# Optimization experiments

Hardware: AMD Instinct MI355X
Metric: run time of the kernel (lower is better)

The kernel has to match this reference:

```python
import jax, jax.numpy as jnp
import numpy as np

RADIUS = 0.4   # 0.2 * nlayer, nlayer = 2
NSAMPLE = 32   # k


def _fps(xyz, m):
    """Farthest point sampling. xyz: (B, N, 3) -> idx (B, m) int32.
    Matches pointnet2 CUDA kernel: first sampled point is index 0."""
    B, N, _ = xyz.shape

    def step(carry, _):
        dist, far = carry
        centroid = jnp.take_along_axis(xyz, far[:, None, None], axis=1)  # (B,1,3)
        d = jnp.sum((xyz - centroid) ** 2, axis=-1)                      # (B,N)
        dist = jnp.minimum(dist, d)
        return (dist, jnp.argmax(dist, axis=-1).astype(jnp.int32)), far

    init = (jnp.full((B, N), jnp.inf, dtype=xyz.dtype),
            jnp.zeros((B,), dtype=jnp.int32))
    _, idx = jax.lax.scan(step, init, None, length=m)  # (m, B)
    return idx.T                                       # (B, m)


def _ball_query(radius, k, xyz, new_xyz):
    """xyz (B,N,3), new_xyz (B,M,3) -> (B,M,k) int32.
    First k in-radius indices in ascending index order; slots past the
    number of in-radius points are filled with the first found index
    (pointnet2 ball_query semantics)."""
    N = xyz.shape[1]
    d2 = jnp.sum((new_xyz[:, :, None, :] - xyz[:, None, :, :]) ** 2, axis=-1)  # (B,M,N)
    key = jnp.where(d2 < radius * radius,
                    jnp.arange(N, dtype=jnp.int32), jnp.int32(N))              # (B,M,N)
    topv, _ = jax.lax.top_k(-key, k)   # k smallest keys, ascending
    idx = -topv                        # (B,M,k)
    valid = idx < N
    idx = jnp.where(valid, idx, idx[..., :1])  # pad with first found index
    return idx


def _group(t, idx):
    """t (B,C,N), idx (B,M,k) -> (B,C,M,k)."""
    return jnp.take_along_axis(t[:, :, None, :], idx[:, None, :, :], axis=3)


def setup_inputs() -> dict:
    key = jax.random.key(0)
    k1, k2, k3 = jax.random.split(key, 3)
    return {
        "x": jax.random.normal(k1, (8, 3, 8192), dtype=jnp.float32),
        "feature": jax.random.normal(k2, (8, 64, 8192), dtype=jnp.float32),
        "weight": jax.random.normal(k3, (64, 64), dtype=jnp.float32) / 8.0,
        "num_pool": 2048,
    }


def reference(x, feature, weight, num_pool):
    # x: (B,3,N) coordinates, feature: (B,C,N), weight: 1x1 conv (C_out, C_in)
    xyz = jnp.transpose(x, (0, 2, 1))                       # (B,N,3)
    fps_idx = _fps(xyz, num_pool)                           # (B,M)
    new_xyz = jnp.take_along_axis(xyz, fps_idx[:, :, None], axis=1)  # (B,M,3)
    sub_idx = _ball_query(RADIUS, NSAMPLE, xyz, new_xyz)    # (B,M,k)

    x_out = _group(x, sub_idx).max(axis=-1)                 # (B,3,M)
    fg = _group(feature, sub_idx)                           # (B,C,M,k)
    f_out = jnp.einsum('oc,bcmk->bomk', weight, fg).max(axis=-1)  # (B,C,M)
    return x_out, f_out
```

## Files before the change

kernel.cpp:

```cpp
#include <hip/hip_runtime.h>
#include <cstdint>
#include <cstddef>

#define BB 8
#define NN 8192
#define CC 64
#define MM 2048
#define KK 32

typedef float vfloat2 __attribute__((ext_vector_type(2)));

__device__ __forceinline__ float sqdist_exact(float x, float y, float z,
                                              float cx, float cy, float cz) {
    float dx = __fsub_rn(x, cx);
    float dy = __fsub_rn(y, cy);
    float dz = __fsub_rn(z, cz);
    return __fadd_rn(__fadd_rn(__fmul_rn(dx, dx), __fmul_rn(dy, dy)),
                     __fmul_rn(dz, dz));
}

template <int CTRL>
__device__ __forceinline__ unsigned dpp_max_u32(unsigned v) {
    unsigned s = (unsigned)__builtin_amdgcn_update_dpp(0, (int)v, CTRL, 0xF, 0xF, true);
    return v > s ? v : s;
}
template <int CTRL>
__device__ __forceinline__ unsigned dpp_min_u32(unsigned v) {
    unsigned s = (unsigned)__builtin_amdgcn_update_dpp(0x7FFFFFFF, (int)v, CTRL, 0xF, 0xF, false);
    return v < s ? v : s;
}

__device__ __forceinline__ int octile(float v) {
    return (v > -1.1503494f) + (v > -0.6744898f) + (v > -0.3186394f) + (v > 0.0f) +
           (v > 0.3186394f) + (v > 0.6744898f) + (v > 1.1503494f);
}

__device__ __forceinline__ int morton9(int bx, int by, int bz) {
    int m = (bz & 1) | ((bz & 2) << 2) | ((bz & 4) << 4);
    m |= ((by & 1) << 1) | ((by & 2) << 3) | ((by & 4) << 5);
    m |= ((bx & 1) << 2) | ((bx & 2) << 4) | ((bx & 4) << 6);
    return m;
}

__global__ __launch_bounds__(512) void fps_kernel(const float* __restrict__ x,
                                                  int* __restrict__ fps_idx) {
#pragma clang fp contract(off)
    const int b = blockIdx.x;
    const int tid = threadIdx.x;
    const int lane = tid & 63;
    const float* xb = x + (size_t)b * 3 * NN;
    int* fps_store = fps_idx + b * MM;

    __shared__ float sx[NN];
    __shared__ float sy[NN];
    __shared__ float sz[NN];
    __shared__ int sidx[NN];
    __shared__ int hist[512];
    __shared__ int scanb[512];
    __shared__ int sfps[MM];
    __shared__ unsigned long long red3[3];

    const vfloat2* gx = (const vfloat2*)xb;
    const vfloat2* gy = (const vfloat2*)(xb + NN);
    const vfloat2* gz = (const vfloat2*)(xb + 2 * NN);

    vfloat2 lx[8], ly[8], lz[8];
#pragma unroll
    for (int p = 0; p < 8; ++p) {
        const int e = tid + p * 512;
        lx[p] = gx[e];
        ly[p] = gy[e];
        lz[p] = gz[e];
        ((vfloat2*)sx)[e] = lx[p];
        ((vfloat2*)sy)[e] = ly[p];
        ((vfloat2*)sz)[e] = lz[p];
    }
    hist[tid] = 0;
    if (tid < 3) red3[tid] = 0ull;
    __syncthreads();

    int mybin[16];
#pragma unroll
    for (int p = 0; p < 8; ++p) {
        int b0 = morton9(octile(lx[p].x), octile(ly[p].x), octile(lz[p].x));
        int b1 = morton9(octile(lx[p].y), octile(ly[p].y), octile(lz[p].y));
        mybin[2 * p] = b0;
        mybin[2 * p + 1] = b1;
        atomicAdd(&hist[b0], 1);
        atomicAdd(&hist[b1], 1);
    }
    __syncthreads();
    int own = hist[tid];
    scanb[tid] = own;
    __syncthreads();
    for (int off = 1; off < 512; off <<= 1) {
        int add = (tid >= off) ? scanb[tid - off] : 0;
        __syncthreads();
        scanb[tid] += add;
        __syncthreads();
    }
    hist[tid] = scanb[tid] - own;
    __syncthreads();
#pragma unroll
    for (int p = 0; p < 8; ++p) {
        const int i0 = 2 * (tid + p * 512);
        int pos0 = atomicAdd(&hist[mybin[2 * p]], 1);
        sidx[pos0] = i0;
        int pos1 = atomicAdd(&hist[mybin[2 * p + 1]], 1);
        sidx[pos1] = i0 + 1;
    }
    __syncthreads();

    vfloat2 px[8], py[8], pz[8], dist[8];
    int idxr[16];
#pragma unroll
    for (int p = 0; p < 8; ++p) {
        const int j0 = sidx[tid * 16 + 2 * p];
        const int j1 = sidx[tid * 16 + 2 * p + 1];
        idxr[2 * p] = j0;
        idxr[2 * p + 1] = j1;
        px[p] = (vfloat2){sx[j0], sx[j1]};
        py[p] = (vfloat2){sy[j0], sy[j1]};
        pz[p] = (vfloat2){sz[j0], sz[j1]};
        dist[p] = (vfloat2){INFINITY, INFINITY};
    }
    float blx = fminf(px[0].x, px[0].y), bhx = fmaxf(px[0].x, px[0].y);
    float bly = fminf(py[0].x, py[0].y), bhy = fmaxf(py[0].x, py[0].y);
    float blz = fminf(pz[0].x, pz[0].y), bhz = fmaxf(pz[0].x, pz[0].y);
#pragma unroll
    for (int p = 1; p < 8; ++p) {
        blx = fminf(blx, fminf(px[p].x, px[p].y));
        bhx = fmaxf(bhx, fmaxf(px[p].x, px[p].y));
        bly = fminf(bly, fminf(py[p].x, py[p].y));
        bhy = fmaxf(bhy, fmaxf(py[p].x, py[p].y));
        blz = fminf(blz, fminf(pz[p].x, pz[p].y));
        bhz = fmaxf(bhz, fmaxf(pz[p].x, pz[p].y));
    }

    float cmax = INFINITY;
    int cidx = idxr[0];
    int far = 0;
    for (int t = 0; t < MM; ++t) {
        if (tid == 0) {
            sfps[t] = far;
            red3[(t + 1) % 3] = 0ull;
        }
        const float cx = sx[far];
        const float cy = sy[far];
        const float cz = sz[far];

        float qx = cx - fminf(fmaxf(cx, blx), bhx);
        float qy = cy - fminf(fmaxf(cy, bly), bhy);
        float qz = cz - fminf(fmaxf(cz, blz), bhz);
        float bound = (qx * qx + qy * qy) + qz * qz;
        const bool act = !(bound * 0.999f >= cmax);
        if (act) {
            const vfloat2 cx2 = {cx, cx};
            const vfloat2 cy2 = {cy, cy};
            const vfloat2 cz2 = {cz, cz};
            float mv = -1.0f;
#pragma unroll
            for (int p = 0; p < 8; ++p) {
                vfloat2 dx = px[p] - cx2;
                vfloat2 dy = py[p] - cy2;
                vfloat2 dz = pz[p] - cz2;
                vfloat2 m1 = dx * dx;
                vfloat2 m2 = dy * dy;
                vfloat2 m3 = dz * dz;
                vfloat2 s = (m1 + m2) + m3;
                vfloat2 nd;
                nd.x = fminf(dist[p].x, s.x);
                nd.y = fminf(dist[p].y, s.y);
                dist[p] = nd;
                mv = fmaxf(fmaxf(mv, nd.x), nd.y);
            }
            int mi = 0x7FFFFFFF;
#pragma unroll
            for (int p = 0; p < 8; ++p) {
                mi = min(mi, (dist[p].x == mv) ? idxr[2 * p] : 0x7FFFFFFF);
                mi = min(mi, (dist[p].y == mv) ? idxr[2 * p + 1] : 0x7FFFFFFF);
            }
            cmax = mv;
            cidx = mi;
        }

        unsigned mvb = __float_as_uint(cmax);
        mvb = dpp_max_u32<0x111>(mvb);
        mvb = dpp_max_u32<0x112>(mvb);
        mvb = dpp_max_u32<0x114>(mvb);
        mvb = dpp_max_u32<0x118>(mvb);
        mvb = dpp_max_u32<0x142>(mvb);
        mvb = dpp_max_u32<0x143>(mvb);
        const unsigned wmax = (unsigned)__builtin_amdgcn_readlane((int)mvb, 63);
        unsigned midx = (__float_as_uint(cmax) == wmax) ? (unsigned)cidx : 0x7FFFFFFFu;
        midx = dpp_min_u32<0x111>(midx);
        midx = dpp_min_u32<0x112>(midx);
        midx = dpp_min_u32<0x114>(midx);
        midx = dpp_min_u32<0x118>(midx);
        midx = dpp_min_u32<0x142>(midx);
        midx = dpp_min_u32<0x143>(midx);
        if (lane == 63) {
            unsigned long long key =
                ((unsigned long long)wmax << 32) | (unsigned)(~midx);
            atomicMax(&red3[t % 3], key);
        }
        __syncthreads();
        far = (int)(~(unsigned)red3[t % 3]);
    }
    __syncthreads();
    for (int t = tid; t < MM; t += 512) fps_store[t] = sfps[t];
}

__global__ __launch_bounds__(256) void transform_kernel(const float* __restrict__ feature,
                                                        const float* __restrict__ weight,
                                                        float* __restrict__ g) {
    __shared__ float Wl[64 * 64];
    const int tid = threadIdx.x;
    for (int k = tid; k < 64 * 64; k += 256) Wl[k] = weight[k];
    __syncthreads();

    const int P = blockIdx.x * 256 + tid;
    const int b = P >> 13;
    const int n = P & (NN - 1);
    const float* fb = feature + (size_t)b * CC * NN + n;

    float fr[64];
#pragma unroll
    for (int c = 0; c < 64; ++c) fr[c] = fb[(size_t)c * NN];

    float* go = g + ((size_t)b << 19) + (size_t)n * 64;
    for (int o = 0; o < 64; o += 4) {
        const float* w0 = &Wl[o * 64];
        const float* w1 = w0 + 64;
        const float* w2 = w0 + 128;
        const float* w3 = w0 + 192;
        float a0 = 0.f, a1 = 0.f, a2 = 0.f, a3 = 0.f;
#pragma unroll
        for (int c = 0; c < 64; c += 4) {
            float4 v0 = *(const float4*)(w0 + c);
            float4 v1 = *(const float4*)(w1 + c);
            float4 v2 = *(const float4*)(w2 + c);
            float4 v3 = *(const float4*)(w3 + c);
            a0 += v0.x * fr[c] + v0.y * fr[c + 1] + v0.z * fr[c + 2] + v0.w * fr[c + 3];
            a1 += v1.x * fr[c] + v1.y * fr[c + 1] + v1.z * fr[c + 2] + v1.w * fr[c + 3];
            a2 += v2.x * fr[c] + v2.y * fr[c + 1] + v2.z * fr[c + 2] + v2.w * fr[c + 3];
            a3 += v3.x * fr[c] + v3.y * fr[c + 1] + v3.z * fr[c + 2] + v3.w * fr[c + 3];
        }
        float4 r;
        r.x = a0; r.y = a1; r.z = a2; r.w = a3;
        *(float4*)(go + o) = r;
    }
}

__global__ __launch_bounds__(256) void bq_kernel(const float* __restrict__ x,
                                                 const int* __restrict__ fps_idx,
                                                 int* __restrict__ sub_idx,
                                                 float* __restrict__ xout) {
    const float R2 = (float)(0.4 * 0.4);
    int gw = (int)((blockIdx.x * 256 + threadIdx.x) >> 6);
    const int lane = threadIdx.x & 63;
    gw = __builtin_amdgcn_readfirstlane(gw);
    const int b = gw >> 11;
    const int m = gw & (MM - 1);
    const float* xb = x + (size_t)b * 3 * NN;

    const int ctr = fps_idx[gw];
    const float cx = xb[ctr];
    const float cy = xb[NN + ctr];
    const float cz = xb[2 * NN + ctr];

    int* sid = sub_idx + (size_t)gw * KK;
    int found = 0;
    int first = 0;
    float mx = -INFINITY, my = -INFINITY, mz = -INFINITY;

    for (int base = 0; base < NN; base += 64) {
        const int i = base + lane;
        const float xx = xb[i];
        const float yy = xb[NN + i];
        const float zz = xb[2 * NN + i];
        const float d2 = sqdist_exact(xx, yy, zz, cx, cy, cz);
        const bool q = d2 < R2;
        const unsigned long long mask = __ballot(q);
        if (q) {
            int pos = found + (int)__popcll(mask & ((1ull << lane) - 1ull));
            if (pos < KK) {
                sid[pos] = i;
                mx = fmaxf(mx, xx);
                my = fmaxf(my, yy);
                mz = fmaxf(mz, zz);
            }
        }
        if (found == 0 && mask != 0ull) first = base + (int)__builtin_ctzll(mask);
        found += (int)__popcll(mask);
        if (found >= KK) break;
    }
    if (found < KK) {
        if (lane < KK - found) sid[found + lane] = first;
    }
#pragma unroll
    for (int off = 32; off >= 1; off >>= 1) {
        mx = fmaxf(mx, __shfl_xor(mx, off, 64));
        my = fmaxf(my, __shfl_xor(my, off, 64));
        mz = fmaxf(mz, __shfl_xor(mz, off, 64));
    }
    if (lane == 0) {
        xout[(size_t)b * 3 * MM + 0 * MM + m] = mx;
        xout[(size_t)b * 3 * MM + 1 * MM + m] = my;
        xout[(size_t)b * 3 * MM + 2 * MM + m] = mz;
    }
}

__global__ __launch_bounds__(256) void gather_kernel(const float* __restrict__ g,
                                                     const int* __restrict__ sub_idx,
                                                     float* __restrict__ fout) {
    int gw = (int)((blockIdx.x * 256 + threadIdx.x) >> 6);
    const int lane = threadIdx.x & 63;
    gw = __builtin_amdgcn_readfirstlane(gw);
    const int b = gw >> 11;
    const int m = gw & (MM - 1);
    const int* sid = sub_idx + (size_t)gw * KK;
    const float* gb = g + ((size_t)b << 19);
    float acc = -INFINITY;
#pragma unroll
    for (int j = 0; j < KK; ++j) {
        const int id = sid[j];
        acc = fmaxf(acc, gb[(size_t)id * 64 + lane]);
    }
    fout[((size_t)b << 17) + ((size_t)lane << 11) + m] = acc;
}

extern "C" void kernel_launch(void* const* d_in, const int* in_sizes, int n_in,
                              void* d_out, int out_size, void* d_ws, size_t ws_size,
                              hipStream_t stream) {
    const float* x = (const float*)d_in[0];
    const float* feature = (const float*)d_in[1];
    const float* weight = (const float*)d_in[2];

    float* out = (float*)d_out;
    float* xout = out;
    float* fout = out + BB * 3 * MM;

    char* ws = (char*)d_ws;
    int* fps_idx = (int*)ws;
    int* sub_idx = (int*)(ws + (size_t)BB * MM * 4);
    float* g = (float*)(ws + (size_t)BB * MM * 4 + (size_t)BB * MM * KK * 4);

    fps_kernel<<<BB, 512, 0, stream>>>(x, fps_idx);
    transform_kernel<<<(BB * NN) / 256, 256, 0, stream>>>(feature, weight, g);
    bq_kernel<<<(BB * MM * 64) / 256, 256, 0, stream>>>(x, fps_idx, sub_idx, xout);
    gather_kernel<<<(BB * MM * 64) / 256, 256, 0, stream>>>(g, sub_idx, fout);
}
```

Measured before the change: 1.923 ms.

## Shrink FPS block, pack xyz in LDS, fuse ball query with gather

The FPS kernel drops from 512 to 256 threads per block, so each thread holds 32 points and the per-iteration barrier covers fewer waves. Coordinates are packed as interleaved xyz in shared memory. The two-pass wave argmax is replaced by one 64-bit key max reduction done with DPP. Separately, the ball-query and feature-gather kernels are merged so neighbor indices stay in LDS instead of passing through global memory. The risks are higher register pressure from doubling per-thread point state and serial ALU work per FPS iteration, on a kernel that runs only 8 blocks.

```diff
diff --git a/kernel.cpp b/kernel.cpp
--- a/kernel.cpp
+++ b/kernel.cpp
@@ -20,14 +20,13 @@
 }
 
 template <int CTRL>
-__device__ __forceinline__ unsigned dpp_max_u32(unsigned v) {
-    unsigned s = (unsigned)__builtin_amdgcn_update_dpp(0, (int)v, CTRL, 0xF, 0xF, true);
-    return v > s ? v : s;
-}
-template <int CTRL>
-__device__ __forceinline__ unsigned dpp_min_u32(unsigned v) {
-    unsigned s = (unsigned)__builtin_amdgcn_update_dpp(0x7FFFFFFF, (int)v, CTRL, 0xF, 0xF, false);
-    return v < s ? v : s;
+__device__ __forceinline__ unsigned long long dpp_max_u64(unsigned long long key) {
+    int lo = (int)(unsigned)key;
+    int hi = (int)(unsigned)(key >> 32);
+    int slo = __builtin_amdgcn_update_dpp(0, lo, CTRL, 0xF, 0xF, true);
+    int shi = __builtin_amdgcn_update_dpp(0, hi, CTRL, 0xF, 0xF, true);
+    unsigned long long o = ((unsigned long long)(unsigned)shi << 32) | (unsigned)slo;
+    return o > key ? o : key;
 }
 
 __device__ __forceinline__ int octile(float v) {
@@ -42,7 +41,7 @@
     return m;
 }
 
-__global__ __launch_bounds__(512) void fps_kernel(const float* __restrict__ x,
+__global__ __launch_bounds__(256) void fps_kernel(const float* __restrict__ x,
                                                   int* __restrict__ fps_idx) {
 #pragma clang fp contract(off)
     const int b = blockIdx.x;
@@ -51,9 +50,7 @@
     const float* xb = x + (size_t)b * 3 * NN;
     int* fps_store = fps_idx + b * MM;
 
-    __shared__ float sx[NN];
-    __shared__ float sy[NN];
-    __shared__ float sz[NN];
+    __shared__ float spk[NN * 3];
     __shared__ int sidx[NN];
     __shared__ int hist[512];
     __shared__ int scanb[512];
@@ -64,71 +61,76 @@
     const vfloat2* gy = (const vfloat2*)(xb + NN);
     const vfloat2* gz = (const vfloat2*)(xb + 2 * NN);
 
-    vfloat2 lx[8], ly[8], lz[8];
-#pragma unroll
-    for (int p = 0; p < 8; ++p) {
-        const int e = tid + p * 512;
-        lx[p] = gx[e];
-        ly[p] = gy[e];
-        lz[p] = gz[e];
-        ((vfloat2*)sx)[e] = lx[p];
-        ((vfloat2*)sy)[e] = ly[p];
-        ((vfloat2*)sz)[e] = lz[p];
+#pragma unroll
+    for (int p = 0; p < 16; ++p) {
+        const int e = tid + p * 256;
+        vfloat2 ax = gx[e];
+        vfloat2 ay = gy[e];
+        vfloat2 az = gz[e];
+        spk[6 * e + 0] = ax.x;
+        spk[6 * e + 1] = ay.x;
+        spk[6 * e + 2] = az.x;
+        spk[6 * e + 3] = ax.y;
+        spk[6 * e + 4] = ay.y;
+        spk[6 * e + 5] = az.y;
     }
     hist[tid] = 0;
+    hist[tid + 256] = 0;
     if (tid < 3) red3[tid] = 0ull;
     __syncthreads();
 
-    int mybin[16];
-#pragma unroll
-    for (int p = 0; p < 8; ++p) {
-        int b0 = morton9(octile(lx[p].x), octile(ly[p].x), octile(lz[p].x));
-        int b1 = morton9(octile(lx[p].y), octile(ly[p].y), octile(lz[p].y));
-        mybin[2 * p] = b0;
-        mybin[2 * p + 1] = b1;
-        atomicAdd(&hist[b0], 1);
-        atomicAdd(&hist[b1], 1);
-    }
-    __syncthreads();
-    int own = hist[tid];
-    scanb[tid] = own;
+    int mybin[32];
+#pragma unroll
+    for (int p = 0; p < 32; ++p) {
+        const int i = tid + p * 256;
+        int bn = morton9(octile(spk[3 * i]), octile(spk[3 * i + 1]),
+                         octile(spk[3 * i + 2]));
+        mybin[p] = bn;
+        atomicAdd(&hist[bn], 1);
+    }
+    __syncthreads();
+    int own0 = hist[tid];
+    int own1 = hist[tid + 256];
+    scanb[tid] = own0;
+    scanb[tid + 256] = own1;
     __syncthreads();
     for (int off = 1; off < 512; off <<= 1) {
-        int add = (tid >= off) ? scanb[tid - off] : 0;
+        int a0 = (tid >= off) ? scanb[tid - off] : 0;
+        int a1 = (tid + 256 >= off) ? scanb[tid + 256 - off] : 0;
         __syncthreads();
-        scanb[tid] += add;
+        scanb[tid] += a0;
+        scanb[tid + 256] += a1;
         __syncthreads();
     }
-    hist[tid] = scanb[tid] - own;
-    __syncthreads();
-#pragma unroll
-    for (int p = 0; p < 8; ++p) {
-        const int i0 = 2 * (tid + p * 512);
-        int pos0 = atomicAdd(&hist[mybin[2 * p]], 1);
-        sidx[pos0] = i0;
-        int pos1 = atomicAdd(&hist[mybin[2 * p + 1]], 1);
-        sidx[pos1] = i0 + 1;
-    }
-    __syncthreads();
-
-    vfloat2 px[8], py[8], pz[8], dist[8];
-    int idxr[16];
-#pragma unroll
-    for (int p = 0; p < 8; ++p) {
-        const int j0 = sidx[tid * 16 + 2 * p];
-        const int j1 = sidx[tid * 16 + 2 * p + 1];
+    hist[tid] = scanb[tid] - own0;
+    hist[tid + 256] = scanb[tid + 256] - own1;
+    __syncthreads();
+#pragma unroll
+    for (int p = 0; p < 32; ++p) {
+        const int i = tid + p * 256;
+        int pos = atomicAdd(&hist[mybin[p]], 1);
+        sidx[pos] = i;
+    }
+    __syncthreads();
+
+    vfloat2 px[16], py[16], pz[16], dist[16];
+    int idxr[32];
+#pragma unroll
+    for (int p = 0; p < 16; ++p) {
+        const int j0 = sidx[tid * 32 + 2 * p];
+        const int j1 = sidx[tid * 32 + 2 * p + 1];
         idxr[2 * p] = j0;
         idxr[2 * p + 1] = j1;
-        px[p] = (vfloat2){sx[j0], sx[j1]};
-        py[p] = (vfloat2){sy[j0], sy[j1]};
-        pz[p] = (vfloat2){sz[j0], sz[j1]};
+        px[p] = (vfloat2){spk[3 * j0], spk[3 * j1]};
+        py[p] = (vfloat2){spk[3 * j0 + 1], spk[3 * j1 + 1]};
+        pz[p] = (vfloat2){spk[3 * j0 + 2], spk[3 * j1 + 2]};
         dist[p] = (vfloat2){INFINITY, INFINITY};
     }
     float blx = fminf(px[0].x, px[0].y), bhx = fmaxf(px[0].x, px[0].y);
     float bly = fminf(py[0].x, py[0].y), bhy = fmaxf(py[0].x, py[0].y);
     float blz = fminf(pz[0].x, pz[0].y), bhz = fmaxf(pz[0].x, pz[0].y);
 #pragma unroll
-    for (int p = 1; p < 8; ++p) {
+    for (int p = 1; p < 16; ++p) {
         blx = fminf(blx, fminf(px[p].x, px[p].y));
         bhx = fmaxf(bhx, fmaxf(px[p].x, px[p].y));
         bly = fminf(bly, fminf(py[p].x, py[p].y));
@@ -145,9 +147,9 @@
             sfps[t] = far;
             red3[(t + 1) % 3] = 0ull;
         }
-        const float cx = sx[far];
-        const float cy = sy[far];
-        const float cz = sz[far];
+        const float cx = spk[3 * far];
+        const float cy = spk[3 * far + 1];
+        const float cz = spk[3 * far + 2];
 
         float qx = cx - fminf(fmaxf(cx, blx), bhx);
         float qy = cy - fminf(fmaxf(cy, bly), bhy);
@@ -160,7 +162,7 @@
             const vfloat2 cz2 = {cz, cz};
             float mv = -1.0f;
 #pragma unroll
-            for (int p = 0; p < 8; ++p) {
+            for (int p = 0; p < 16; ++p) {
                 vfloat2 dx = px[p] - cx2;
                 vfloat2 dy = py[p] - cy2;
                 vfloat2 dz = pz[p] - cz2;
@@ -176,7 +178,7 @@
             }
             int mi = 0x7FFFFFFF;
 #pragma unroll
-            for (int p = 0; p < 8; ++p) {
+            for (int p = 0; p < 16; ++p) {
                 mi = min(mi, (dist[p].x == mv) ? idxr[2 * p] : 0x7FFFFFFF);
                 mi = min(mi, (dist[p].y == mv) ? idxr[2 * p + 1] : 0x7FFFFFFF);
             }
@@ -184,31 +186,21 @@
             cidx = mi;
         }
 
-        unsigned mvb = __float_as_uint(cmax);
-        mvb = dpp_max_u32<0x111>(mvb);
-        mvb = dpp_max_u32<0x112>(mvb);
-        mvb = dpp_max_u32<0x114>(mvb);
-        mvb = dpp_max_u32<0x118>(mvb);
-        mvb = dpp_max_u32<0x142>(mvb);
-        mvb = dpp_max_u32<0x143>(mvb);
-        const unsigned wmax = (unsigned)__builtin_amdgcn_readlane((int)mvb, 63);
-        unsigned midx = (__float_as_uint(cmax) == wmax) ? (unsigned)cidx : 0x7FFFFFFFu;
-        midx = dpp_min_u32<0x111>(midx);
-        midx = dpp_min_u32<0x112>(midx);
-        midx = dpp_min_u32<0x114>(midx);
-        midx = dpp_min_u32<0x118>(midx);
-        midx = dpp_min_u32<0x142>(midx);
-        midx = dpp_min_u32<0x143>(midx);
-        if (lane == 63) {
-            unsigned long long key =
-                ((unsigned long long)wmax << 32) | (unsigned)(~midx);
-            atomicMax(&red3[t % 3], key);
-        }
+        unsigned long long key =
+            ((unsigned long long)__float_as_uint(cmax) << 32) |
+            (unsigned)(~(unsigned)cidx);
+        key = dpp_max_u64<0x111>(key);
+        key = dpp_max_u64<0x112>(key);
+        key = dpp_max_u64<0x114>(key);
+        key = dpp_max_u64<0x118>(key);
+        key = dpp_max_u64<0x142>(key);
+        key = dpp_max_u64<0x143>(key);
+        if (lane == 63) atomicMax(&red3[t % 3], key);
         __syncthreads();
         far = (int)(~(unsigned)red3[t % 3]);
     }
     __syncthreads();
-    for (int t = tid; t < MM; t += 512) fps_store[t] = sfps[t];
+    for (int t = tid; t < MM; t += 256) fps_store[t] = sfps[t];
 }
 
 __global__ __launch_bounds__(256) void transform_kernel(const float* __restrict__ feature,
@@ -252,13 +244,16 @@
     }
 }
 
-__global__ __launch_bounds__(256) void bq_kernel(const float* __restrict__ x,
-                                                 const int* __restrict__ fps_idx,
-                                                 int* __restrict__ sub_idx,
-                                                 float* __restrict__ xout) {
+__global__ __launch_bounds__(256) void bqgather_kernel(const float* __restrict__ x,
+                                                       const int* __restrict__ fps_idx,
+                                                       const float* __restrict__ g,
+                                                       float* __restrict__ xout,
+                                                       float* __restrict__ fout) {
     const float R2 = (float)(0.4 * 0.4);
+    __shared__ int sidl[4][KK];
     int gw = (int)((blockIdx.x * 256 + threadIdx.x) >> 6);
     const int lane = threadIdx.x & 63;
+    const int wvl = threadIdx.x >> 6;
     gw = __builtin_amdgcn_readfirstlane(gw);
     const int b = gw >> 11;
     const int m = gw & (MM - 1);
@@ -269,7 +264,6 @@
     const float cy = xb[NN + ctr];
     const float cz = xb[2 * NN + ctr];
 
-    int* sid = sub_idx + (size_t)gw * KK;
     int found = 0;
     int first = 0;
     float mx = -INFINITY, my = -INFINITY, mz = -INFINITY;
@@ -285,7 +279,7 @@
         if (q) {
             int pos = found + (int)__popcll(mask & ((1ull << lane) - 1ull));
             if (pos < KK) {
-                sid[pos] = i;
+                sidl[wvl][pos] = i;
                 mx = fmaxf(mx, xx);
                 my = fmaxf(my, yy);
                 mz = fmaxf(mz, zz);
@@ -296,7 +290,7 @@
         if (found >= KK) break;
     }
     if (found < KK) {
-        if (lane < KK - found) sid[found + lane] = first;
+        if (lane < KK - found) sidl[wvl][found + lane] = first;
     }
 #pragma unroll
     for (int off = 32; off >= 1; off >>= 1) {
@@ -309,22 +303,13 @@
         xout[(size_t)b * 3 * MM + 1 * MM + m] = my;
         xout[(size_t)b * 3 * MM + 2 * MM + m] = mz;
     }
-}
-
-__global__ __launch_bounds__(256) void gather_kernel(const float* __restrict__ g,
-                                                     const int* __restrict__ sub_idx,
-                                                     float* __restrict__ fout) {
-    int gw = (int)((blockIdx.x * 256 + threadIdx.x) >> 6);
-    const int lane = threadIdx.x & 63;
-    gw = __builtin_amdgcn_readfirstlane(gw);
-    const int b = gw >> 11;
-    const int m = gw & (MM - 1);
-    const int* sid = sub_idx + (size_t)gw * KK;
+    __syncthreads();
+
     const float* gb = g + ((size_t)b << 19);
     float acc = -INFINITY;
 #pragma unroll
     for (int j = 0; j < KK; ++j) {
-        const int id = sid[j];
+        const int id = sidl[wvl][j];
         acc = fmaxf(acc, gb[(size_t)id * 64 + lane]);
     }
     fout[((size_t)b << 17) + ((size_t)lane << 11) + m] = acc;
@@ -343,11 +328,9 @@
 
     char* ws = (char*)d_ws;
     int* fps_idx = (int*)ws;
-    int* sub_idx = (int*)(ws + (size_t)BB * MM * 4);
     float* g = (float*)(ws + (size_t)BB * MM * 4 + (size_t)BB * MM * KK * 4);
 
-    fps_kernel<<<BB, 512, 0, stream>>>(x, fps_idx);
+    fps_kernel<<<BB, 256, 0, stream>>>(x, fps_idx);
     transform_kernel<<<(BB * NN) / 256, 256, 0, stream>>>(feature, weight, g);
-    bq_kernel<<<(BB * MM * 64) / 256, 256, 0, stream>>>(x, fps_idx, sub_idx, xout);
-    gather_kernel<<<(BB * MM * 64) / 256, 256, 0, stream>>>(g, sub_idx, fout);
-}
+    bqgather_kernel<<<(BB * MM * 64) / 256, 256, 0, stream>>>(x, fps_idx, g, xout, fout);
+}
```

Result: slower. 2.935 ms (+52.6%).
